# Performance work log

Hardware: AMD Instinct MI355X
Metric: run time of the kernel (lower is better)

## Reference

```python
import jax, jax.numpy as jnp
import numpy as np

B, N, FH, H, FO = 8, 1024, 128, 8, 64
FIN = 2 * FH  # f_hid * 2
NEG = -1e9
SLOPE = 0.2  # leaky_relu negative slope (GAT default)


def setup_inputs() -> dict:
    key = jax.random.key(0)
    ks = jax.random.split(key, 10)
    x = jax.random.normal(ks[0], (B, FIN), jnp.float32)
    A = jax.random.randint(ks[1], (B, N, N), 0, 2, jnp.int32)  # 0/1 dense adjacency
    mask_zero = jnp.ones((B, N, 1), jnp.float32)  # node validity mask
    p_atten = jax.random.uniform(ks[2], (B, N), jnp.float32)  # unused in forward body
    e_atten = jax.random.uniform(ks[3], (B, N, FIN), jnp.float32)
    Npost = jax.random.normal(ks[4], (N, FIN), jnp.float32) * np.float32(1.0 / np.sqrt(FIN))  # kaiming-ish
    w = jax.random.normal(ks[5], (H, FIN, FO), jnp.float32) * np.float32(1.0 / np.sqrt(FIN))
    a_src = jax.random.normal(ks[6], (H, FO), jnp.float32) * np.float32(0.1)
    a_dst = jax.random.normal(ks[7], (H, FO), jnp.float32) * np.float32(0.1)
    bias = jnp.zeros((FO,), jnp.float32)
    return {"x": x, "A": A, "mask_zero": mask_zero, "p_atten": p_atten,
            "e_atten": e_atten, "Npost": Npost, "w": w, "a_src": a_src,
            "a_dst": a_dst, "bias": bias}


def reference(x, A, mask_zero, p_atten, e_atten, Npost, w, a_src, a_dst, bias):
    # broadcast-mul feature gating: x [B,FIN] repeated over N posts, gated by Npost*e_atten
    recx = x[:, None, :] * (Npost[None, :, :] * e_atten)          # [B,N,FIN]
    # BatchGAT (DeepInf-style multi-head graph attention, dropout disabled / eval mode)
    h = jnp.einsum('bnf,hfo->bhno', recx, w)                      # [B,H,N,FO]
    s = jnp.einsum('bhno,ho->bhn', h, a_src)                      # src attention term
    d = jnp.einsum('bhno,ho->bhn', h, a_dst)                      # dst attention term
    logits = jax.nn.leaky_relu(s[:, :, :, None] + d[:, :, None, :], SLOPE)  # [B,H,N,N]
    adj = (A > 0)[:, None, :, :]                                  # [B,1,N,N]
    logits = jnp.where(adj, logits, NEG)
    attn = jax.nn.softmax(logits, axis=-1)                        # masked row softmax
    out = jnp.einsum('bhnm,bhmo->bhno', attn, h) + bias           # aggregate neighbors
    out = out.mean(axis=1)                                        # average heads -> [B,N,FO]
    return out * mask_zero                                        # zero padded nodes
```

## Files before the change

kernel.cpp:

```cpp
#include <hip/hip_runtime.h>

typedef __attribute__((ext_vector_type(8))) short          bf16x8;
typedef __attribute__((ext_vector_type(8))) unsigned short u16x8;
typedef __attribute__((ext_vector_type(4))) unsigned short u16x4;
typedef __attribute__((ext_vector_type(4))) float          f32x4;
typedef __attribute__((ext_vector_type(4))) unsigned int   u32x4;

union U8 { u16x8 u; bf16x8 b; u32x4 w; };
union U4 { u16x4 u; unsigned w[2]; };

__device__ __forceinline__ unsigned short f2bf(float f){
  unsigned u = __float_as_uint(f);
  return (unsigned short)((u + 0x7fffu + ((u >> 16) & 1u)) >> 16);
}
__device__ __forceinline__ unsigned pack_bf16(float lo, float hi){
  unsigned a = __float_as_uint(hi) + 0x8000u;
  unsigned b = __float_as_uint(lo) + 0x8000u;
  return __builtin_amdgcn_perm(a, b, 0x07060302u);
}

#define NN  1024
#define FIN 256
#define NH  8
#define FO  64

__global__ __launch_bounds__(256) void stage0(
    const float* __restrict__ x, const float* __restrict__ e_at,
    const float* __restrict__ Np, const float* __restrict__ w,
    const int* __restrict__ A,
    unsigned short* __restrict__ recx, unsigned short* __restrict__ wB,
    unsigned long long* __restrict__ Abits)
{
  const int tid = blockIdx.x * 256 + threadIdx.x;
  {
    const int g = tid;
    const int f8 = (g & 31) * 8;
    const int n  = (g >> 5) & 1023;
    const int b  = g >> 15;
    const float* ep = e_at + (b * NN + n) * FIN + f8;
    const float* qp = Np + n * FIN + f8;
    const float* xp = x + b * FIN + f8;
    f32x4 e0 = *(const f32x4*)ep, e1 = *(const f32x4*)(ep + 4);
    f32x4 q0 = *(const f32x4*)qp, q1 = *(const f32x4*)(qp + 4);
    f32x4 x0 = *(const f32x4*)xp, x1 = *(const f32x4*)(xp + 4);
    u16x8 r;
    #pragma unroll
    for (int j = 0; j < 4; j++){
      r[j]     = f2bf(e0[j] * q0[j] * x0[j]);
      r[j + 4] = f2bf(e1[j] * q1[j] * x1[j]);
    }
    *(u16x8*)(recx + g * 8) = r;
  }
  if (tid < 131072){
    const int o = tid & 63, f = (tid >> 6) & 255, h = tid >> 14;
    wB[h * 16384 + o * FIN + f] = f2bf(w[tid]);
  }
  for (int i = tid; i < 8388608; i += 262144){
    unsigned long long m = __ballot(A[i] > 0);
    if ((threadIdx.x & 63) == 0) Abits[i >> 6] = m;
  }
}

__global__ __launch_bounds__(512, 2) void stageA(
    const unsigned short* __restrict__ recx,
    const unsigned short* __restrict__ wB,
    const float* __restrict__ a_src, const float* __restrict__ a_dst,
    unsigned short* __restrict__ hT,
    float* __restrict__ exps, float* __restrict__ exps2,
    float* __restrict__ expd, float* __restrict__ expd2)
{
  const int t = threadIdx.x;
  const int n0 = blockIdx.x * 32, b = blockIdx.y;
  const int h = t >> 6, lane = t & 63, quad = lane >> 4, l15 = lane & 15;

  const unsigned short* ap0 = recx + (b * NN + n0 + l15) * FIN + quad * 8;
  const unsigned short* ap1 = ap0 + 16 * FIN;
  const unsigned short* wp  = wB + h * 16384 + l15 * FIN + quad * 8;

  f32x4 acc[2][4] = {};
  #pragma unroll
  for (int kc = 0; kc < 8; kc++){
    U8 a0, a1, bf[4];
    a0.u = *(const u16x8*)(ap0 + kc * 32);
    a1.u = *(const u16x8*)(ap1 + kc * 32);
    #pragma unroll
    for (int ss = 0; ss < 4; ss++) bf[ss].u = *(const u16x8*)(wp + ss * 16 * FIN + kc * 32);
    #pragma unroll
    for (int ss = 0; ss < 4; ss++)
      acc[0][ss] = __builtin_amdgcn_mfma_f32_16x16x32_bf16(a0.b, bf[ss].b, acc[0][ss], 0, 0, 0);
    #pragma unroll
    for (int ss = 0; ss < 4; ss++)
      acc[1][ss] = __builtin_amdgcn_mfma_f32_16x16x32_bf16(a1.b, bf[ss].b, acc[1][ss], 0, 0, 0);
  }

  {
    unsigned short* pan = hT + (size_t)(((b * NH + h) * 32 + (n0 >> 5)) * 64) * 32;
    #pragma unroll
    for (int rg = 0; rg < 2; rg++)
      #pragma unroll
      for (int ss = 0; ss < 4; ss++){
        U4 v;
        v.w[0] = pack_bf16(acc[rg][ss][0], acc[rg][ss][1]);
        v.w[1] = pack_bf16(acc[rg][ss][2], acc[rg][ss][3]);
        *(u16x4*)(pan + (16 * ss + l15) * 32 + rg * 16 + quad * 4) = v.u;
      }
  }

  float as4[4], ad4[4];
  #pragma unroll
  for (int ss = 0; ss < 4; ss++){
    as4[ss] = a_src[h * FO + 16 * ss + l15];
    ad4[ss] = a_dst[h * FO + 16 * ss + l15];
  }
  #pragma unroll
  for (int rg = 0; rg < 2; rg++)
    #pragma unroll
    for (int i = 0; i < 4; i++){
      float ps = 0.f, pd = 0.f;
      #pragma unroll
      for (int ss = 0; ss < 4; ss++){ ps += acc[rg][ss][i] * as4[ss]; pd += acc[rg][ss][i] * ad4[ss]; }
      #pragma unroll
      for (int off = 1; off < 16; off <<= 1){
        ps += __shfl_xor(ps, off);
        pd += __shfl_xor(pd, off);
      }
      if (l15 == 0){
        const int idx = (b * NH + h) * NN + n0 + rg * 16 + quad * 4 + i;
        exps [idx] = __expf(ps);
        exps2[idx] = __expf(0.2f * ps);
        expd [idx] = __expf(pd);
        expd2[idx] = __expf(0.2f * pd);
      }
    }
}

__global__ __launch_bounds__(1024, 4) void stageB(
    const unsigned* __restrict__ Aw,
    const unsigned short* __restrict__ hT,
    const float* __restrict__ exps, const float* __restrict__ exps2,
    const float* __restrict__ expd, const float* __restrict__ expd2,
    const float* __restrict__ bias, const float* __restrict__ mz,
    float* __restrict__ out)
{
  __shared__ float ed_l[NH * NN];
  __shared__ float e2_l[NH * NN];
  __shared__ unsigned mask_l[32 * 33];
  __shared__ float oacc[32 * 65];
  const int t = threadIdx.x, b = blockIdx.y, n0 = blockIdx.x * 32;
  const int h = (t >> 6) & 7, rg = t >> 9;
  const int lane = t & 63, quad = lane >> 4, l15 = lane & 15;
  const int row = n0 + rg * 16 + l15;

  for (int i = t; i < 32 * 65; i += 1024) oacc[i] = 0.f;
  {
    const float* s1 = expd  + b * 8192;
    const float* s2 = expd2 + b * 8192;
    *(f32x4*)(ed_l + t * 4)        = *(const f32x4*)(s1 + t * 4);
    *(f32x4*)(ed_l + t * 4 + 4096) = *(const f32x4*)(s1 + t * 4 + 4096);
    *(f32x4*)(e2_l + t * 4)        = *(const f32x4*)(s2 + t * 4);
    *(f32x4*)(e2_l + t * 4 + 4096) = *(const f32x4*)(s2 + t * 4 + 4096);
  }
  mask_l[(t >> 5) * 33 + (t & 31)] = Aw[(b * NN + n0 + (t >> 5)) * 32 + (t & 31)];
  __syncthreads();

  const float Es  = exps [(b * NH + h) * NN + row];
  const float Es2 = exps2[(b * NH + h) * NN + row];
  const unsigned short* pb = hT + (size_t)(b * NH + h) * 65536 + l15 * 32 + quad * 8;
  const float* edh = ed_l + h * NN + quad * 8;
  const float* e2h = e2_l + h * NN + quad * 8;
  const int mrow = (rg * 16 + l15) * 33;

  U8 ones;
  #pragma unroll
  for (int j = 0; j < 8; j++) ones.u[j] = 0x3F80;

  U8 b0[4], b1[4];
  #pragma unroll
  for (int ss = 0; ss < 4; ss++){
    b0[ss].u = *(const u16x8*)(pb + ss * 512);
    b1[ss].u = *(const u16x8*)(pb + 2048 + ss * 512);
  }

  f32x4 acc[4] = {}, accs = {};

  for (int c = 0; c < 32; c++){
    U8 cur[4];
    #pragma unroll
    for (int ss = 0; ss < 4; ss++){ cur[ss] = b0[ss]; b0[ss] = b1[ss]; }
    if (c + 2 < 32){
      #pragma unroll
      for (int ss = 0; ss < 4; ss++)
        b1[ss].u = *(const u16x8*)(pb + (c + 2) * 2048 + ss * 512);
    }
    const unsigned abyte = mask_l[mrow + c] >> (quad * 8);
    f32x4 d0 = *(const f32x4*)(edh + c * 32);
    f32x4 d1 = *(const f32x4*)(edh + c * 32 + 4);
    f32x4 g0 = *(const f32x4*)(e2h + c * 32);
    f32x4 g1 = *(const f32x4*)(e2h + c * 32 + 4);
    U8 p;
    #pragma unroll
    for (int r = 0; r < 4; r++){
      const int j0 = 2 * r, j1 = 2 * r + 1;
      const float dj0 = (j0 < 4) ? d0[j0] : d1[j0 - 4];
      const float gj0 = (j0 < 4) ? g0[j0] : g1[j0 - 4];
      const float dj1 = (j1 < 4) ? d0[j1] : d1[j1 - 4];
      const float gj1 = (j1 < 4) ? g0[j1] : g1[j1 - 4];
      float e0 = fmaxf(Es * dj0, Es2 * gj0);
      float e1 = fmaxf(Es * dj1, Es2 * gj1);
      e0 = (abyte & (1u << j0)) ? e0 : 0.f;
      e1 = (abyte & (1u << j1)) ? e1 : 0.f;
      p.w[r] = pack_bf16(e0, e1);
    }
    #pragma unroll
    for (int ss = 0; ss < 4; ss++)
      acc[ss] = __builtin_amdgcn_mfma_f32_16x16x32_bf16(p.b, cur[ss].b, acc[ss], 0, 0, 0);
    accs = __builtin_amdgcn_mfma_f32_16x16x32_bf16(p.b, ones.b, accs, 0, 0, 0);
  }

  float inv[4];
  #pragma unroll
  for (int i = 0; i < 4; i++) inv[i] = 0.125f / accs[i];

  #pragma unroll
  for (int ss = 0; ss < 4; ss++)
    #pragma unroll
    for (int i = 0; i < 4; i++)
      atomicAdd(&oacc[(rg * 16 + quad * 4 + i) * 65 + ss * 16 + l15], acc[ss][i] * inv[i]);
  __syncthreads();

  for (int i = t; i < 2048; i += 1024){
    const int r = i >> 6, o = i & 63;
    out[(b * NN + n0 + r) * FO + o] = (oacc[r * 65 + o] + bias[o]) * mz[b * NN + n0 + r];
  }
}

extern "C" void kernel_launch(void* const* d_in, const int* in_sizes, int n_in,
                              void* d_out, int out_size, void* d_ws, size_t ws_size,
                              hipStream_t stream)
{
  (void)in_sizes; (void)n_in; (void)out_size; (void)ws_size;
  const float* x    = (const float*)d_in[0];
  const int*   A    = (const int*)d_in[1];
  const float* mz   = (const float*)d_in[2];
  const float* e_at = (const float*)d_in[4];
  const float* Np   = (const float*)d_in[5];
  const float* w    = (const float*)d_in[6];
  const float* asrc = (const float*)d_in[7];
  const float* adst = (const float*)d_in[8];
  const float* bias = (const float*)d_in[9];
  float* out = (float*)d_out;

  char* ws = (char*)d_ws;
  unsigned short* recx = (unsigned short*)ws;
  unsigned short* wBuf = (unsigned short*)(ws + 4194304);
  unsigned short* hT   = (unsigned short*)(ws + 4456448);
  float* exps  = (float*)(ws + 12845056);
  float* exps2 = (float*)(ws + 13107200);
  float* expd  = (float*)(ws + 13369344);
  float* expd2 = (float*)(ws + 13631488);
  unsigned long long* Abits = (unsigned long long*)(ws + 13893632);

  stage0<<<dim3(1024), dim3(256), 0, stream>>>(x, e_at, Np, w, A, recx, wBuf, Abits);
  stageA<<<dim3(32, 8), dim3(512), 0, stream>>>(recx, wBuf, asrc, adst, hT,
                                                exps, exps2, expd, expd2);
  stageB<<<dim3(32, 8), dim3(1024), 0, stream>>>((const unsigned*)Abits, hT,
                                                 exps, exps2, expd, expd2,
                                                 bias, mz, out);
}
```

Before: 175.2 us.

## Fuse recx gating into stageA via LDS and split stageB over key halves

The elementwise recx gating (x*Npost*e_atten converted to bf16) moves from stage0 into stageA, where each block builds its 32-row tile in shared memory. This removes the 4 MB recx workspace round trip. The weights are pre-laid out in MFMA fragment order so stageA loads them contiguously. stageB now has each warp cover both 16-row groups over half of the key columns, so every loaded hT panel feeds two row groups. Row sums are combined across the halves with shared-memory atomics before normalising. The trade-off is more registers per thread in stageB and an extra barrier.

```diff
diff --git a/kernel.cpp b/kernel.cpp
--- a/kernel.cpp
+++ b/kernel.cpp
@@ -25,35 +25,18 @@
 #define FO  64
 
 __global__ __launch_bounds__(256) void stage0(
-    const float* __restrict__ x, const float* __restrict__ e_at,
-    const float* __restrict__ Np, const float* __restrict__ w,
-    const int* __restrict__ A,
-    unsigned short* __restrict__ recx, unsigned short* __restrict__ wB,
-    unsigned long long* __restrict__ Abits)
+    const float* __restrict__ w, const int* __restrict__ A,
+    unsigned short* __restrict__ wfrag, unsigned long long* __restrict__ Abits)
 {
   const int tid = blockIdx.x * 256 + threadIdx.x;
-  {
-    const int g = tid;
-    const int f8 = (g & 31) * 8;
-    const int n  = (g >> 5) & 1023;
-    const int b  = g >> 15;
-    const float* ep = e_at + (b * NN + n) * FIN + f8;
-    const float* qp = Np + n * FIN + f8;
-    const float* xp = x + b * FIN + f8;
-    f32x4 e0 = *(const f32x4*)ep, e1 = *(const f32x4*)(ep + 4);
-    f32x4 q0 = *(const f32x4*)qp, q1 = *(const f32x4*)(qp + 4);
-    f32x4 x0 = *(const f32x4*)xp, x1 = *(const f32x4*)(xp + 4);
+  if (tid < 16384){
+    const int lane = tid & 63, ss = (tid >> 6) & 3, kc = (tid >> 8) & 7, h = tid >> 11;
+    const int o = 16 * ss + (lane & 15);
+    const int f = kc * 32 + (lane >> 4) * 8;
     u16x8 r;
     #pragma unroll
-    for (int j = 0; j < 4; j++){
-      r[j]     = f2bf(e0[j] * q0[j] * x0[j]);
-      r[j + 4] = f2bf(e1[j] * q1[j] * x1[j]);
-    }
-    *(u16x8*)(recx + g * 8) = r;
-  }
-  if (tid < 131072){
-    const int o = tid & 63, f = (tid >> 6) & 255, h = tid >> 14;
-    wB[h * 16384 + o * FIN + f] = f2bf(w[tid]);
+    for (int j = 0; j < 8; j++) r[j] = f2bf(w[(h * FIN + f + j) * FO + o]);
+    *(u16x8*)(wfrag + tid * 8) = r;
   }
   for (int i = tid; i < 8388608; i += 262144){
     unsigned long long m = __ballot(A[i] > 0);
@@ -61,30 +44,51 @@
   }
 }
 
-__global__ __launch_bounds__(512, 2) void stageA(
-    const unsigned short* __restrict__ recx,
-    const unsigned short* __restrict__ wB,
+__global__ __launch_bounds__(512, 4) void stageA(
+    const float* __restrict__ x, const float* __restrict__ e_at,
+    const float* __restrict__ Np, const unsigned short* __restrict__ wfrag,
     const float* __restrict__ a_src, const float* __restrict__ a_dst,
     unsigned short* __restrict__ hT,
     float* __restrict__ exps, float* __restrict__ exps2,
     float* __restrict__ expd, float* __restrict__ expd2)
 {
+  __shared__ unsigned short rex[32 * 264];
   const int t = threadIdx.x;
   const int n0 = blockIdx.x * 32, b = blockIdx.y;
+
+  {
+    const int row = t >> 4, f0 = (t & 15) * 16;
+    const int nrow = n0 + row;
+    const float* ep = e_at + (b * NN + nrow) * FIN + f0;
+    const float* qp = Np + nrow * FIN + f0;
+    const float* xp = x + b * FIN + f0;
+    #pragma unroll
+    for (int g = 0; g < 2; g++){
+      f32x4 e0 = *(const f32x4*)(ep + g * 8), e1 = *(const f32x4*)(ep + g * 8 + 4);
+      f32x4 q0 = *(const f32x4*)(qp + g * 8), q1 = *(const f32x4*)(qp + g * 8 + 4);
+      f32x4 x0 = *(const f32x4*)(xp + g * 8), x1 = *(const f32x4*)(xp + g * 8 + 4);
+      u16x8 r;
+      #pragma unroll
+      for (int j = 0; j < 4; j++){
+        r[j]     = f2bf(e0[j] * q0[j] * x0[j]);
+        r[j + 4] = f2bf(e1[j] * q1[j] * x1[j]);
+      }
+      *(u16x8*)(rex + row * 264 + f0 + g * 8) = r;
+    }
+  }
+  __syncthreads();
+
   const int h = t >> 6, lane = t & 63, quad = lane >> 4, l15 = lane & 15;
-
-  const unsigned short* ap0 = recx + (b * NN + n0 + l15) * FIN + quad * 8;
-  const unsigned short* ap1 = ap0 + 16 * FIN;
-  const unsigned short* wp  = wB + h * 16384 + l15 * FIN + quad * 8;
+  const unsigned short* wf = wfrag + h * 16384 + lane * 8;
 
   f32x4 acc[2][4] = {};
   #pragma unroll
   for (int kc = 0; kc < 8; kc++){
     U8 a0, a1, bf[4];
-    a0.u = *(const u16x8*)(ap0 + kc * 32);
-    a1.u = *(const u16x8*)(ap1 + kc * 32);
-    #pragma unroll
-    for (int ss = 0; ss < 4; ss++) bf[ss].u = *(const u16x8*)(wp + ss * 16 * FIN + kc * 32);
+    a0.u = *(const u16x8*)(rex + l15 * 264 + kc * 32 + quad * 8);
+    a1.u = *(const u16x8*)(rex + (16 + l15) * 264 + kc * 32 + quad * 8);
+    #pragma unroll
+    for (int ss = 0; ss < 4; ss++) bf[ss].u = *(const u16x8*)(wf + (kc * 4 + ss) * 512);
     #pragma unroll
     for (int ss = 0; ss < 4; ss++)
       acc[0][ss] = __builtin_amdgcn_mfma_f32_16x16x32_bf16(a0.b, bf[ss].b, acc[0][ss], 0, 0, 0);
@@ -134,6 +138,45 @@
     }
 }
 
+#define PCHUNK(C, PAN)                                                          \
+  {                                                                             \
+    const int c_ = (C);                                                         \
+    const unsigned w0_ = mask_l[l15 * 33 + c_];                                 \
+    const unsigned w1_ = mask_l[(16 + l15) * 33 + c_];                          \
+    const unsigned ab0_ = w0_ >> (quad * 8), ab1_ = w1_ >> (quad * 8);          \
+    f32x4 d0_ = *(const f32x4*)(edh + c_ * 32);                                 \
+    f32x4 d1_ = *(const f32x4*)(edh + c_ * 32 + 4);                             \
+    f32x4 g0_ = *(const f32x4*)(e2h + c_ * 32);                                 \
+    f32x4 g1_ = *(const f32x4*)(e2h + c_ * 32 + 4);                             \
+    U8 p0_, p1_;                                                                \
+    _Pragma("unroll")                                                           \
+    for (int r_ = 0; r_ < 4; r_++){                                             \
+      const int j0_ = 2 * r_, j1_ = 2 * r_ + 1;                                 \
+      const float dj0_ = (j0_ < 4) ? d0_[j0_] : d1_[j0_ - 4];                   \
+      const float gj0_ = (j0_ < 4) ? g0_[j0_] : g1_[j0_ - 4];                   \
+      const float dj1_ = (j1_ < 4) ? d0_[j1_] : d1_[j1_ - 4];                   \
+      const float gj1_ = (j1_ < 4) ? g0_[j1_] : g1_[j1_ - 4];                   \
+      float e00_ = fmaxf(Es0 * dj0_, Es20 * gj0_);                              \
+      float e01_ = fmaxf(Es0 * dj1_, Es20 * gj1_);                              \
+      float e10_ = fmaxf(Es1 * dj0_, Es21 * gj0_);                              \
+      float e11_ = fmaxf(Es1 * dj1_, Es21 * gj1_);                              \
+      e00_ = (ab0_ & (1u << j0_)) ? e00_ : 0.f;                                 \
+      e01_ = (ab0_ & (1u << j1_)) ? e01_ : 0.f;                                 \
+      e10_ = (ab1_ & (1u << j0_)) ? e10_ : 0.f;                                 \
+      e11_ = (ab1_ & (1u << j1_)) ? e11_ : 0.f;                                 \
+      p0_.w[r_] = pack_bf16(e00_, e01_);                                        \
+      p1_.w[r_] = pack_bf16(e10_, e11_);                                        \
+    }                                                                           \
+    _Pragma("unroll")                                                           \
+    for (int ss_ = 0; ss_ < 4; ss_++)                                           \
+      acc[0][ss_] = __builtin_amdgcn_mfma_f32_16x16x32_bf16(p0_.b, PAN[ss_].b, acc[0][ss_], 0, 0, 0); \
+    accs[0] = __builtin_amdgcn_mfma_f32_16x16x32_bf16(p0_.b, ones.b, accs[0], 0, 0, 0); \
+    _Pragma("unroll")                                                           \
+    for (int ss_ = 0; ss_ < 4; ss_++)                                           \
+      acc[1][ss_] = __builtin_amdgcn_mfma_f32_16x16x32_bf16(p1_.b, PAN[ss_].b, acc[1][ss_], 0, 0, 0); \
+    accs[1] = __builtin_amdgcn_mfma_f32_16x16x32_bf16(p1_.b, ones.b, accs[1], 0, 0, 0); \
+  }
+
 __global__ __launch_bounds__(1024, 4) void stageB(
     const unsigned* __restrict__ Aw,
     const unsigned short* __restrict__ hT,
@@ -145,13 +188,14 @@
   __shared__ float ed_l[NH * NN];
   __shared__ float e2_l[NH * NN];
   __shared__ unsigned mask_l[32 * 33];
+  __shared__ float l_l[NH * 32];
   __shared__ float oacc[32 * 65];
   const int t = threadIdx.x, b = blockIdx.y, n0 = blockIdx.x * 32;
-  const int h = (t >> 6) & 7, rg = t >> 9;
+  const int h = (t >> 6) & 7, mh = t >> 9;
   const int lane = t & 63, quad = lane >> 4, l15 = lane & 15;
-  const int row = n0 + rg * 16 + l15;
 
   for (int i = t; i < 32 * 65; i += 1024) oacc[i] = 0.f;
+  if (t < NH * 32) l_l[t] = 0.f;
   {
     const float* s1 = expd  + b * 8192;
     const float* s2 = expd2 + b * 8192;
@@ -163,69 +207,64 @@
   mask_l[(t >> 5) * 33 + (t & 31)] = Aw[(b * NN + n0 + (t >> 5)) * 32 + (t & 31)];
   __syncthreads();
 
-  const float Es  = exps [(b * NH + h) * NN + row];
-  const float Es2 = exps2[(b * NH + h) * NN + row];
+  const int hb = (b * NH + h) * NN;
+  const float Es0  = exps [hb + n0 + l15],      Es20 = exps2[hb + n0 + l15];
+  const float Es1  = exps [hb + n0 + 16 + l15], Es21 = exps2[hb + n0 + 16 + l15];
   const unsigned short* pb = hT + (size_t)(b * NH + h) * 65536 + l15 * 32 + quad * 8;
   const float* edh = ed_l + h * NN + quad * 8;
   const float* e2h = e2_l + h * NN + quad * 8;
-  const int mrow = (rg * 16 + l15) * 33;
+  const int c0 = mh * 16;
 
   U8 ones;
   #pragma unroll
   for (int j = 0; j < 8; j++) ones.u[j] = 0x3F80;
 
-  U8 b0[4], b1[4];
+  U8 pan0[4], pan1[4];
   #pragma unroll
   for (int ss = 0; ss < 4; ss++){
-    b0[ss].u = *(const u16x8*)(pb + ss * 512);
-    b1[ss].u = *(const u16x8*)(pb + 2048 + ss * 512);
-  }
-
-  f32x4 acc[4] = {}, accs = {};
-
-  for (int c = 0; c < 32; c++){
-    U8 cur[4];
-    #pragma unroll
-    for (int ss = 0; ss < 4; ss++){ cur[ss] = b0[ss]; b0[ss] = b1[ss]; }
-    if (c + 2 < 32){
+    pan0[ss].u = *(const u16x8*)(pb + (size_t)c0 * 2048 + ss * 512);
+    pan1[ss].u = *(const u16x8*)(pb + (size_t)(c0 + 1) * 2048 + ss * 512);
+  }
+
+  f32x4 acc[2][4] = {};
+  f32x4 accs[2] = {};
+
+  for (int cc = 0; cc < 16; cc += 2){
+    PCHUNK(c0 + cc, pan0)
+    if (cc + 2 < 16){
       #pragma unroll
       for (int ss = 0; ss < 4; ss++)
-        b1[ss].u = *(const u16x8*)(pb + (c + 2) * 2048 + ss * 512);
+        pan0[ss].u = *(const u16x8*)(pb + (size_t)(c0 + cc + 2) * 2048 + ss * 512);
     }
-    const unsigned abyte = mask_l[mrow + c] >> (quad * 8);
-    f32x4 d0 = *(const f32x4*)(edh + c * 32);
-    f32x4 d1 = *(const f32x4*)(edh + c * 32 + 4);
-    f32x4 g0 = *(const f32x4*)(e2h + c * 32);
-    f32x4 g1 = *(const f32x4*)(e2h + c * 32 + 4);
-    U8 p;
-    #pragma unroll
-    for (int r = 0; r < 4; r++){
-      const int j0 = 2 * r, j1 = 2 * r + 1;
-      const float dj0 = (j0 < 4) ? d0[j0] : d1[j0 - 4];
-      const float gj0 = (j0 < 4) ? g0[j0] : g1[j0 - 4];
-      const float dj1 = (j1 < 4) ? d0[j1] : d1[j1 - 4];
-      const float gj1 = (j1 < 4) ? g0[j1] : g1[j1 - 4];
-      float e0 = fmaxf(Es * dj0, Es2 * gj0);
-      float e1 = fmaxf(Es * dj1, Es2 * gj1);
-      e0 = (abyte & (1u << j0)) ? e0 : 0.f;
-      e1 = (abyte & (1u << j1)) ? e1 : 0.f;
-      p.w[r] = pack_bf16(e0, e1);
+    PCHUNK(c0 + cc + 1, pan1)
+    if (cc + 3 < 16){
+      #pragma unroll
+      for (int ss = 0; ss < 4; ss++)
+        pan1[ss].u = *(const u16x8*)(pb + (size_t)(c0 + cc + 3) * 2048 + ss * 512);
     }
+  }
+
+  if (l15 == 0){
+    #pragma unroll
+    for (int rg = 0; rg < 2; rg++)
+      #pragma unroll
+      for (int i = 0; i < 4; i++)
+        atomicAdd(&l_l[h * 32 + rg * 16 + quad * 4 + i], accs[rg][i]);
+  }
+  __syncthreads();
+
+  #pragma unroll
+  for (int rg = 0; rg < 2; rg++){
+    float inv[4];
+    #pragma unroll
+    for (int i = 0; i < 4; i++)
+      inv[i] = 0.125f / l_l[h * 32 + rg * 16 + quad * 4 + i];
     #pragma unroll
     for (int ss = 0; ss < 4; ss++)
-      acc[ss] = __builtin_amdgcn_mfma_f32_16x16x32_bf16(p.b, cur[ss].b, acc[ss], 0, 0, 0);
-    accs = __builtin_amdgcn_mfma_f32_16x16x32_bf16(p.b, ones.b, accs, 0, 0, 0);
-  }
-
-  float inv[4];
-  #pragma unroll
-  for (int i = 0; i < 4; i++) inv[i] = 0.125f / accs[i];
-
-  #pragma unroll
-  for (int ss = 0; ss < 4; ss++)
-    #pragma unroll
-    for (int i = 0; i < 4; i++)
-      atomicAdd(&oacc[(rg * 16 + quad * 4 + i) * 65 + ss * 16 + l15], acc[ss][i] * inv[i]);
+      #pragma unroll
+      for (int i = 0; i < 4; i++)
+        atomicAdd(&oacc[(rg * 16 + quad * 4 + i) * 65 + ss * 16 + l15], acc[rg][ss][i] * inv[i]);
+  }
   __syncthreads();
 
   for (int i = t; i < 2048; i += 1024){
@@ -251,18 +290,17 @@
   float* out = (float*)d_out;
 
   char* ws = (char*)d_ws;
-  unsigned short* recx = (unsigned short*)ws;
-  unsigned short* wBuf = (unsigned short*)(ws + 4194304);
-  unsigned short* hT   = (unsigned short*)(ws + 4456448);
-  float* exps  = (float*)(ws + 12845056);
-  float* exps2 = (float*)(ws + 13107200);
-  float* expd  = (float*)(ws + 13369344);
-  float* expd2 = (float*)(ws + 13631488);
-  unsigned long long* Abits = (unsigned long long*)(ws + 13893632);
-
-  stage0<<<dim3(1024), dim3(256), 0, stream>>>(x, e_at, Np, w, A, recx, wBuf, Abits);
-  stageA<<<dim3(32, 8), dim3(512), 0, stream>>>(recx, wBuf, asrc, adst, hT,
-                                                exps, exps2, expd, expd2);
+  unsigned short* wfrag = (unsigned short*)ws;
+  unsigned short* hT    = (unsigned short*)(ws + 262144);
+  float* exps  = (float*)(ws + 8650752);
+  float* exps2 = (float*)(ws + 8912896);
+  float* expd  = (float*)(ws + 9175040);
+  float* expd2 = (float*)(ws + 9437184);
+  unsigned long long* Abits = (unsigned long long*)(ws + 9699328);
+
+  stage0<<<dim3(1024), dim3(256), 0, stream>>>(w, A, wfrag, Abits);
+  stageA<<<dim3(32, 8), dim3(512), 0, stream>>>(x, e_at, Np, wfrag, asrc, adst,
+                                                hT, exps, exps2, expd, expd2);
   stageB<<<dim3(32, 8), dim3(1024), 0, stream>>>((const unsigned*)Abits, hT,
                                                  exps, exps2, expd, expd2,
                                                  bias, mz, out);
```

Result: no change. 177.6 us (+1.4%).
